# Kernel tuning notes

Hardware: AMD Instinct MI355X
Metric: run time of the kernel (lower is better)

Reference implementation:

```python
import jax, jax.numpy as jnp
import numpy as np

NFFT = 512
NFILT = 40
EPS = float(np.finfo(np.float64).eps)  # np.finfo(float).eps in the original


def _mel_fbank(fs: int, nfft: int = NFFT, nfilt: int = NFILT) -> np.ndarray:
    # Faithful reconstruction of the original triangular filterbank,
    # including int() truncation of bin edges and the (j+1) offsets.
    high_freq_mel = 2595.0 * np.log10(1.0 + fs / 2.0 / 700.0)
    mel_points = np.linspace(0.0, high_freq_mel, nfilt + 2)
    hz_points = 700.0 * (10.0 ** (mel_points / 2595.0) - 1.0)
    b = hz_points / (fs / 2.0) * (nfft / 2.0)
    fbank = np.zeros((nfilt, nfft // 2 + 1), dtype=np.float64)
    for i in range(1, nfilt + 1):
        left, center, right = int(b[i - 1]), int(b[i]), int(b[i + 1])
        for j in range(left, center):
            fbank[i - 1, j + 1] = (j + 1 - b[i - 1]) / (b[i] - b[i - 1])
        for j in range(center, right):
            fbank[i - 1, j + 1] = (b[i + 1] - (j + 1)) / (b[i + 1] - b[i])
    return fbank.astype(np.float32)


def setup_inputs() -> dict:
    key = jax.random.key(0)
    Signals = jax.random.normal(key, (32, 50000), dtype=jnp.float32)
    return {"Signals": Signals, "fs": 1000}


def reference(Signals, fs):
    # NOTE: in the original, Signal = Signals[i].unsqueeze(0) makes the
    # pre-emphasis slice arithmetic operate on an empty array, so the
    # "emphasized" signal is just the raw signal. The hamming window is
    # computed but never applied. Both bugs replicated faithfully.
    B, L = Signals.shape
    frame_length = int(round(0.025 * fs))   # 25
    frame_step = int(round(0.01 * fs))      # 10
    num_frames = int(np.ceil(abs(L - frame_length) / frame_step)) + 1
    pad_len = (num_frames - 1) * frame_step + frame_length

    padded = jnp.pad(Signals, ((0, 0), (0, pad_len - L)))  # [B, pad_len]
    # static frame-gather indices [num_frames, frame_length]
    idx = (np.arange(frame_length)[None, :]
           + np.arange(0, num_frames * frame_step, frame_step)[:, None])
    frames = padded[:, idx]                                # [B, T, frame_length]

    mag = jnp.abs(jnp.fft.rfft(frames, NFFT))              # [B, T, NFFT//2+1]
    pow_frames = mag * mag * (1.0 / NFFT)

    fbank = jnp.asarray(_mel_fbank(fs))                    # [nfilt, NFFT//2+1]
    fb = jnp.einsum('btf,nf->btn', pow_frames, fbank)      # [B, T, nfilt]
    fb = jnp.where(fb == 0, EPS, fb)
    return (20.0 * jnp.log10(fb)).astype(jnp.float32)
```

## Files before the change

kernel.cpp:

```cpp
#include <hip/hip_runtime.h>

#define NFILT   40
#define FLEN    25
#define FSTEP   10
#define BATCH   32
#define SIGLEN  50000
#define NFRAMES 4999
#define EPSV    2.220446049250313e-16f
#define TPB     256
#define SPAN4   2576
#define OSTR    41

namespace ctab {

constexpr double PI   = 3.14159265358979323846264338327950288;
constexpr double LN10 = 2.30258509299404568401799145468436421;

constexpr double cln(double y) {
    double z = (y - 1.0) / (y + 1.0);
    double z2 = z * z, term = z, s = 0.0;
    for (int k = 0; k < 40; ++k) { s += term / (2.0 * k + 1.0); term *= z2; }
    return 2.0 * s;
}
constexpr double cexp(double x) {
    double s = 1.0, term = 1.0;
    for (int i = 1; i <= 24; ++i) { term *= x / (double)i; s += term; }
    return s;
}
constexpr double ccospi_r(double t) {
    double x = PI * t, x2 = x * x;
    double s = 1.0, term = 1.0;
    for (int k = 1; k <= 16; ++k) { term *= -x2 / ((2.0 * k - 1.0) * (2.0 * k)); s += term; }
    return s;
}
constexpr double ccospi_m(int m) {
    int mm = m & 511;
    if (mm > 256) mm = 512 - mm;
    if (mm <= 128) return ccospi_r(mm / 256.0);
    return -ccospi_r((256 - mm) / 256.0);
}

struct CTab {
    float c[NFILT][FLEN];
    constexpr CTab() : c{} {
        double ct[512] = {};
        for (int m = 0; m < 512; ++m) ct[m] = ccospi_m(m);
        double fs = 1000.0;
        double high_mel = 2595.0 * (cln(1.0 + fs / 2.0 / 700.0) / LN10);
        double b[NFILT + 2] = {};
        for (int i = 0; i < NFILT + 2; ++i) {
            double mel = high_mel * (double)i / (double)(NFILT + 1);
            double hz  = 700.0 * (cexp(mel / 2595.0 * LN10) - 1.0);
            b[i] = hz / (fs / 2.0) * 256.0;
        }
        for (int f = 0; f < NFILT; ++f) {
            int left = (int)b[f], center = (int)b[f + 1], right = (int)b[f + 2];
            for (int d = 0; d < FLEN; ++d) {
                double acc = 0.0;
                for (int j = left; j < right; ++j) {
                    double w = (j < center)
                        ? ((double)(j + 1) - b[f])     / (b[f + 1] - b[f])
                        : (b[f + 2] - (double)(j + 1)) / (b[f + 2] - b[f + 1]);
                    acc += w * ct[((j + 1) * d) & 511];
                }
                double v = acc / 512.0;
                if (d) v *= 2.0;
                c[f][d] = (float)v;
            }
        }
    }
};
static constexpr CTab CT{};

}

__global__ __launch_bounds__(TPB) void mel_main(const float* __restrict__ sig,
                                                float* __restrict__ out) {
    const int b   = blockIdx.y;
    const int t0  = blockIdx.x * TPB;
    const int tid = threadIdx.x;

    __shared__ float s_sig[SPAN4];
    __shared__ float s_stage[128 * OSTR];

    const int base = t0 * FSTEP;
    const int rem  = SIGLEN - base;
    const float* sb = sig + (size_t)b * SIGLEN + base;
    for (int i = tid * 4; i < SPAN4; i += TPB * 4) {
        float4 v = make_float4(0.f, 0.f, 0.f, 0.f);
        if (i + 4 <= rem) {
            v = *reinterpret_cast<const float4*>(sb + i);
        } else if (i < rem) {
            v.x = sb[i];
            if (i + 1 < rem) v.y = sb[i + 1];
            if (i + 2 < rem) v.z = sb[i + 2];
        }
        *reinterpret_cast<float4*>(s_sig + i) = v;
    }
    __syncthreads();

    float x[FLEN];
    const float* sp = s_sig + tid * FSTEP;
    #pragma unroll
    for (int n = 0; n < FLEN; ++n) x[n] = sp[n];

    float R[FLEN];
    #pragma unroll
    for (int d = 0; d < FLEN; ++d) {
        float a = 0.f;
        #pragma unroll
        for (int n = 0; n + d < FLEN; ++n) a = fmaf(x[n], x[n + d], a);
        R[d] = a;
    }

    float fbv[NFILT];
    #pragma unroll
    for (int f = 0; f < NFILT; ++f) {
        float a = 0.f;
        #pragma unroll
        for (int d = 0; d < FLEN; ++d)
            a = fmaf(ctab::CT.c[f][d], R[d], a);
        if (a < EPSV) a = EPSV;
        fbv[f] = 6.0205999132796239f * __log2f(a);
    }

    const size_t outbase = ((size_t)b * NFRAMES + t0) * NFILT;
    #pragma unroll 1
    for (int r = 0; r < 2; ++r) {
        __syncthreads();
        if ((tid >> 7) == r) {
            int lt = tid & 127;
            #pragma unroll
            for (int f = 0; f < NFILT; ++f)
                s_stage[lt * OSTR + f] = fbv[f];
        }
        __syncthreads();
        const int f0 = t0 + r * 128;
        #pragma unroll
        for (int j = 0; j < 20; ++j) {
            int i  = j * TPB + tid;
            int fr = i / 40;
            int fl = i - fr * 40;
            if (f0 + fr < NFRAMES)
                out[outbase + (size_t)r * (128 * NFILT) + i] = s_stage[fr * OSTR + fl];
        }
    }
}

extern "C" void kernel_launch(void* const* d_in, const int* in_sizes, int n_in,
                              void* d_out, int out_size, void* d_ws, size_t ws_size,
                              hipStream_t stream) {
    const float* sig = (const float*)d_in[0];
    float* out = (float*)d_out;
    dim3 grid((NFRAMES + TPB - 1) / TPB, BATCH);
    mel_main<<<grid, dim3(TPB), 0, stream>>>(sig, out);
}
```

Measured before the change: 20.01 us.

## Halve block size, write staged results directly, vectorize output stores

Cuts blocks to 128 threads (40 blocks per batch row) so one staging pass replaces the two-round register-to-shared handoff, and the filter results go straight into shared memory with no register array. Output is written with float4 stores instead of scalar stores, and the launch bound asks for three blocks per CU. The goals are more blocks for better occupancy and wider global writes. The trade-off is more blocks overall and a slightly larger overlap of halo loads per block.

```diff
diff --git a/kernel.cpp b/kernel.cpp
--- a/kernel.cpp
+++ b/kernel.cpp
@@ -7,8 +7,9 @@
 #define SIGLEN  50000
 #define NFRAMES 4999
 #define EPSV    2.220446049250313e-16f
-#define TPB     256
-#define SPAN4   2576
+#define TPB     128
+#define NBLK    40
+#define SPAN4   1296
 #define OSTR    41
 
 namespace ctab {
@@ -74,18 +75,19 @@
 
 }
 
-__global__ __launch_bounds__(TPB) void mel_main(const float* __restrict__ sig,
-                                                float* __restrict__ out) {
+__global__ __launch_bounds__(TPB, 3) void mel_main(const float* __restrict__ sig,
+                                                   float* __restrict__ out) {
     const int b   = blockIdx.y;
     const int t0  = blockIdx.x * TPB;
     const int tid = threadIdx.x;
 
     __shared__ float s_sig[SPAN4];
-    __shared__ float s_stage[128 * OSTR];
+    __shared__ float s_stage[TPB * OSTR];
 
     const int base = t0 * FSTEP;
     const int rem  = SIGLEN - base;
     const float* sb = sig + (size_t)b * SIGLEN + base;
+    #pragma unroll
     for (int i = tid * 4; i < SPAN4; i += TPB * 4) {
         float4 v = make_float4(0.f, 0.f, 0.f, 0.f);
         if (i + 4 <= rem) {
@@ -113,7 +115,7 @@
         R[d] = a;
     }
 
-    float fbv[NFILT];
+    float* st = s_stage + tid * OSTR;
     #pragma unroll
     for (int f = 0; f < NFILT; ++f) {
         float a = 0.f;
@@ -121,28 +123,20 @@
         for (int d = 0; d < FLEN; ++d)
             a = fmaf(ctab::CT.c[f][d], R[d], a);
         if (a < EPSV) a = EPSV;
-        fbv[f] = 6.0205999132796239f * __log2f(a);
+        st[f] = 6.0205999132796239f * __log2f(a);
     }
+    __syncthreads();
 
     const size_t outbase = ((size_t)b * NFRAMES + t0) * NFILT;
-    #pragma unroll 1
-    for (int r = 0; r < 2; ++r) {
-        __syncthreads();
-        if ((tid >> 7) == r) {
-            int lt = tid & 127;
-            #pragma unroll
-            for (int f = 0; f < NFILT; ++f)
-                s_stage[lt * OSTR + f] = fbv[f];
-        }
-        __syncthreads();
-        const int f0 = t0 + r * 128;
-        #pragma unroll
-        for (int j = 0; j < 20; ++j) {
-            int i  = j * TPB + tid;
-            int fr = i / 40;
-            int fl = i - fr * 40;
-            if (f0 + fr < NFRAMES)
-                out[outbase + (size_t)r * (128 * NFILT) + i] = s_stage[fr * OSTR + fl];
+    #pragma unroll
+    for (int j = 0; j < 10; ++j) {
+        int i4 = j * TPB + tid;
+        int fr = i4 / 10;
+        int fl = i4 - fr * 10;
+        if (t0 + fr < NFRAMES) {
+            const float* q = s_stage + fr * OSTR + fl * 4;
+            float4 v = make_float4(q[0], q[1], q[2], q[3]);
+            *reinterpret_cast<float4*>(out + outbase + (size_t)i4 * 4) = v;
         }
     }
 }
@@ -152,6 +146,6 @@
                               hipStream_t stream) {
     const float* sig = (const float*)d_in[0];
     float* out = (float*)d_out;
-    dim3 grid((NFRAMES + TPB - 1) / TPB, BATCH);
+    dim3 grid(NBLK, BATCH);
     mel_main<<<grid, dim3(TPB), 0, stream>>>(sig, out);
 }
```

Result: faster. 18.26 us (-8.8%).
